# Kernel optimization log

Measured on AMD Instinct MI355X. Metric: run time of the kernel, lower is better.

Reference implementation:

```python
import jax, jax.numpy as jnp
import numpy as np

# ---- Clifford algebra G(3,0,1) (projective GA) blade tables, built once in numpy ----
_BLADES = [(), (0,), (1,), (2,), (3,), (0, 1), (0, 2), (0, 3), (1, 2), (1, 3), (2, 3), (0, 1, 2), (0, 1, 3), (0, 2, 3), (1, 2, 3), (0, 1, 2, 3)]
_IDX = {b: i for i, b in enumerate(_BLADES)}
_METRIC = [0.0, 1.0, 1.0, 1.0]  # e0^2 = 0 (degenerate), e1..e3 square to +1

def _blade_mul(a, b):
    arr = list(a) + list(b)
    sign = 1.0
    swapped = True
    while swapped:  # bubble sort, tracking permutation sign
        swapped = False
        for j in range(len(arr) - 1):
            if arr[j] > arr[j + 1]:
                arr[j], arr[j + 1] = arr[j + 1], arr[j]
                sign = -sign
                swapped = True
    res = []
    j = 0
    while j < len(arr):
        if j + 1 < len(arr) and arr[j] == arr[j + 1]:
            sign *= _METRIC[arr[j]]
            j += 2
        else:
            res.append(arr[j])
            j += 1
    return sign, tuple(res)

_GP = np.zeros((16, 16, 16), np.float32)    # geometric product Cayley table
_WEDGE = np.zeros((16, 16, 16), np.float32)  # outer (wedge) product table
for _i, _a in enumerate(_BLADES):
    for _j, _b in enumerate(_BLADES):
        _s, _r = _blade_mul(_a, _b)
        if _s != 0.0:
            _GP[_i, _j, _IDX[_r]] = _s
        if set(_a).isdisjoint(_b):
            _WEDGE[_i, _j, _IDX[_r]] = _s

# dual = right complement: e_a ^ dual(e_a) = e0123 (metric-free, valid in degenerate PGA)
_D = np.zeros((16, 16), np.float32)
for _i, _a in enumerate(_BLADES):
    _comp = tuple(sorted(set(range(4)) - set(_a)))
    _D[_i, _IDX[_comp]] = _WEDGE[_i, _IDX[_comp], 15]
_UND = np.linalg.inv(_D).astype(np.float32)
# join(x, y) = undual(dual(x) ^ dual(y)) as a single 16^3 trilinear table
_JOIN = np.einsum('ia,jb,abc,ck->ijk', _D, _D, _WEDGE, _UND).astype(np.float32)
_GRADES = np.array([len(b) for b in _BLADES])

GP_T = jnp.asarray(_GP)
JOIN_T = jnp.asarray(_JOIN)
GRADES = jnp.asarray(_GRADES)


def _equilin(x, w):
    # Equivariant linear layer: one channel-mixing matrix per grade.
    # x: [B, N, Cin, 16], w: [5, Cout, Cin] -> [B, N, Cout, 16]
    wk = w[GRADES]  # [16, Cout, Cin]
    return jnp.einsum('bnik,koi->bnok', x, wk)


def setup_inputs() -> dict:
    key = jax.random.key(0)
    ks = jax.random.split(key, 7)
    B, N, Cin, Cout = 32, 1024, 64, 64
    H = Cout // 2
    s_in = 1.0 / np.sqrt(Cin)
    s_out = 1.0 / np.sqrt(Cout)
    return {
        'x': jax.random.normal(ks[0], (B, N, Cin, 16), jnp.float32),
        'ref': jax.random.normal(ks[1], (B, N, 16), jnp.float32),
        'w_prodX': jax.random.normal(ks[2], (5, H, Cin), jnp.float32) * s_in,
        'w_prodY': jax.random.normal(ks[3], (5, H, Cin), jnp.float32) * s_in,
        'w_joinX': jax.random.normal(ks[4], (5, H, Cin), jnp.float32) * s_in,
        'w_joinY': jax.random.normal(ks[5], (5, H, Cin), jnp.float32) * s_in,
        'w_final': jax.random.normal(ks[6], (5, Cout, Cout), jnp.float32) * s_out,
    }


def reference(x, ref, w_prodX, w_prodY, w_joinX, w_joinY, w_final):
    # geometric product branch
    px = _equilin(x, w_prodX)
    py = _equilin(x, w_prodY)
    prod = jnp.einsum('bnci,bncj,ijk->bnck', px, py, GP_T)
    # equivariant join branch, scaled by reference pseudoscalar coefficient (GATr)
    jx = _equilin(x, w_joinX)
    jy = _equilin(x, w_joinY)
    join = jnp.einsum('bnci,bncj,ijk->bnck', jx, jy, JOIN_T)
    join = join * ref[..., 15][..., None, None]
    feats = jnp.concatenate([prod, join], axis=-2)  # [B, N, Cout, 16]
    return _equilin(feats, w_final)
```

## Files before the change

### kernel.cpp

```cpp
#include <hip/hip_runtime.h>
#include <stdint.h>


#define BN 32768
#define PLANE 1160
#define TROW 72

typedef __attribute__((ext_vector_type(8))) short short8;
typedef __attribute__((ext_vector_type(4))) float f32x4;

#define MFMA_BF16 __builtin_amdgcn_mfma_f32_16x16x32_bf16

constexpr int IDX2MASK[16] = {0,1,2,4,8,3,5,9,6,10,12,7,11,13,14,15};
constexpr int MASK2IDX[16] = {0,1,2,5,3,6,8,11,4,7,9,12,10,13,14,15};

struct MulRes { float s; int idx; };

constexpr MulRes blade_mul(int ia, int ib) {
  int arr[8] = {0,0,0,0,0,0,0,0}; int n = 0;
  for (int e = 0; e < 4; ++e) if ((IDX2MASK[ia] >> e) & 1) arr[n++] = e;
  for (int e = 0; e < 4; ++e) if ((IDX2MASK[ib] >> e) & 1) arr[n++] = e;
  float sign = 1.0f;
  bool sw = true;
  while (sw) {
    sw = false;
    for (int j = 0; j + 1 < n; ++j)
      if (arr[j] > arr[j+1]) { int t = arr[j]; arr[j] = arr[j+1]; arr[j+1] = t; sign = -sign; sw = true; }
  }
  int mask = 0; int j = 0;
  while (j < n) {
    if (j + 1 < n && arr[j] == arr[j+1]) { if (arr[j] == 0) sign = 0.0f; j += 2; }
    else { mask |= 1 << arr[j]; ++j; }
  }
  return MulRes{sign, MASK2IDX[mask]};
}

constexpr float dual_sign(int i) {
  return blade_mul(i, MASK2IDX[15 ^ IDX2MASK[i]]).s;
}

struct Tab { float s[16][16]; int k[16][16]; };

constexpr Tab make_gp() {
  Tab t{};
  for (int i = 0; i < 16; ++i)
    for (int j = 0; j < 16; ++j) { MulRes r = blade_mul(i, j); t.s[i][j] = r.s; t.k[i][j] = r.idx; }
  return t;
}

constexpr Tab make_join() {
  Tab t{};
  for (int i = 0; i < 16; ++i)
    for (int j = 0; j < 16; ++j) {
      int ma = 15 ^ IDX2MASK[i], mb = 15 ^ IDX2MASK[j];
      if (ma & mb) { t.s[i][j] = 0.0f; t.k[i][j] = 0; continue; }
      int ia = MASK2IDX[ma], ib = MASK2IDX[mb];
      MulRes w = blade_mul(ia, ib);
      int kk = MASK2IDX[15 ^ IDX2MASK[w.idx]];
      t.s[i][j] = dual_sign(i) * dual_sign(j) * w.s * dual_sign(kk);
      t.k[i][j] = kk;
    }
  return t;
}

constexpr Tab GPT = make_gp();
constexpr Tab JNT = make_join();
constexpr int GRADE[16] = {0,1,1,1,1,2,2,2,2,2,2,3,3,3,3,4};

struct KTab { int cnt[16]; int ti[16][16]; int tj[16][16]; float ts[16][16]; };
constexpr KTab make_ktab(const Tab& t) {
  KTab b{};
  for (int i = 0; i < 16; ++i)
    for (int j = 0; j < 16; ++j) {
      float s = t.s[i][j];
      if (s != 0.f) { int k = t.k[i][j]; int m = b.cnt[k]; b.cnt[k] = m + 1;
                      b.ti[k][m] = i; b.tj[k][m] = j; b.ts[k][m] = s; }
    }
  return b;
}
constexpr KTab GPK = make_ktab(GPT);
constexpr KTab JNK = make_ktab(JNT);

__device__ __forceinline__ uint32_t f2bf(float f){
  union{float f; uint32_t i;} v; v.f = f;
  return (v.i + 0x7fffu + ((v.i >> 16) & 1u)) >> 16;
}

__device__ short g_wpre_b[4 * 5 * 32 * 64];
__device__ short g_wfin_b[5 * 64 * 64];

__global__ void cast_weights(const float* __restrict__ wpx, const float* __restrict__ wpy,
                             const float* __restrict__ wjx, const float* __restrict__ wjy,
                             const float* __restrict__ wf) {
  int idx = blockIdx.x * 256 + threadIdx.x;
  if (idx < 40960) {
    int which = idx / 10240, r = idx % 10240;
    const float* src = (which == 0) ? wpx : (which == 1) ? wpy : (which == 2) ? wjx : wjy;
    g_wpre_b[idx] = (short)f2bf(src[r]);
  } else if (idx < 40960 + 20480) {
    int r = idx - 40960;
    g_wfin_b[r] = (short)f2bf(wf[r]);
  }
}

__global__ __launch_bounds__(256, 2) void gbl_kernel(
    const float* __restrict__ x,
    const float* __restrict__ ref,
    float* __restrict__ out)
{
  __shared__ __align__(16) short ldsb[16 * PLANE];

  const int tid  = threadIdx.x;
  const int w    = tid >> 6;
  const int lane = tid & 63;
  const int n    = lane & 15;
  const int q    = lane >> 4;
  const int t0   = blockIdx.x * 16;

  {
    const int k  = tid & 15;
    const int tt = tid >> 4;
    const float* xr = x + (size_t)(t0 + tt) * 1024 + k;
    #pragma unroll
    for (int ib = 0; ib < 8; ++ib) {
      float v[8];
      #pragma unroll
      for (int j = 0; j < 8; ++j) v[j] = xr[(ib * 8 + j) * 16];
      short8 p;
      #pragma unroll
      for (int j = 0; j < 8; ++j) p[j] = (short)f2bf(v[j]);
      *(short8*)&ldsb[k * PLANE + tt * TROW + ib * 8] = p;
    }
  }
  __syncthreads();

  const int br = w >> 1, nt = w & 1;

  float px[16][4], py[16][4];

  {
    short8 B[5][2];
    #pragma unroll
    for (int g = 0; g < 5; ++g)
      #pragma unroll
      for (int ks = 0; ks < 2; ++ks)
        B[g][ks] = *(short8*)&g_wpre_b[(((br * 2 + 0) * 5 + g) * 32 + nt * 16 + n) * 64 + ks * 32 + q * 8];
    #pragma unroll
    for (int kb = 0; kb < 16; ++kb) {
      short8 a0 = *(short8*)&ldsb[kb * PLANE + n * TROW + 0  + q * 8];
      short8 a1 = *(short8*)&ldsb[kb * PLANE + n * TROW + 32 + q * 8];
      f32x4 acc = {0.f, 0.f, 0.f, 0.f};
      acc = MFMA_BF16(a0, B[GRADE[kb]][0], acc, 0, 0, 0);
      acc = MFMA_BF16(a1, B[GRADE[kb]][1], acc, 0, 0, 0);
      #pragma unroll
      for (int r = 0; r < 4; ++r) px[kb][r] = acc[r];
    }
  }
  {
    short8 B[5][2];
    #pragma unroll
    for (int g = 0; g < 5; ++g)
      #pragma unroll
      for (int ks = 0; ks < 2; ++ks)
        B[g][ks] = *(short8*)&g_wpre_b[(((br * 2 + 1) * 5 + g) * 32 + nt * 16 + n) * 64 + ks * 32 + q * 8];
    #pragma unroll
    for (int kb = 0; kb < 16; ++kb) {
      short8 a0 = *(short8*)&ldsb[kb * PLANE + n * TROW + 0  + q * 8];
      short8 a1 = *(short8*)&ldsb[kb * PLANE + n * TROW + 32 + q * 8];
      f32x4 acc = {0.f, 0.f, 0.f, 0.f};
      acc = MFMA_BF16(a0, B[GRADE[kb]][0], acc, 0, 0, 0);
      acc = MFMA_BF16(a1, B[GRADE[kb]][1], acc, 0, 0, 0);
      #pragma unroll
      for (int r = 0; r < 4; ++r) py[kb][r] = acc[r];
    }
  }

  __syncthreads();

  {
    float rv[4];
    if (br == 1) {
      #pragma unroll
      for (int r = 0; r < 4; ++r) rv[r] = ref[(size_t)(t0 + 4 * q + r) * 16 + 15];
    }
    const int cg = w * 16 + n;
    #pragma unroll
    for (int k = 0; k < 16; ++k) {
      float a[4] = {0.f, 0.f, 0.f, 0.f};
      if (br == 0) {
        #pragma unroll
        for (int m = 0; m < 16; ++m) {
          if (m < GPK.cnt[k]) {
            const int i = GPK.ti[k][m], j = GPK.tj[k][m];
            const bool neg = GPK.ts[k][m] < 0.f;
            #pragma unroll
            for (int r = 0; r < 4; ++r)
              a[r] = fmaf(neg ? -px[i][r] : px[i][r], py[j][r], a[r]);
          }
        }
      } else {
        #pragma unroll
        for (int m = 0; m < 16; ++m) {
          if (m < JNK.cnt[k]) {
            const int i = JNK.ti[k][m], j = JNK.tj[k][m];
            const bool neg = JNK.ts[k][m] < 0.f;
            #pragma unroll
            for (int r = 0; r < 4; ++r)
              a[r] = fmaf(neg ? -px[i][r] : px[i][r], py[j][r], a[r]);
          }
        }
        #pragma unroll
        for (int r = 0; r < 4; ++r) a[r] *= rv[r];
      }
      #pragma unroll
      for (int r = 0; r < 4; ++r)
        ldsb[k * PLANE + (4 * q + r) * TROW + cg] = (short)f2bf(a[r]);
    }
  }
  __syncthreads();

  {
    short8 BF[5][2];
    #pragma unroll
    for (int g = 0; g < 5; ++g)
      #pragma unroll
      for (int ks = 0; ks < 2; ++ks)
        BF[g][ks] = *(short8*)&g_wfin_b[(g * 64 + w * 16 + n) * 64 + ks * 32 + q * 8];

    f32x4 D[16];
    #pragma unroll
    for (int kb = 0; kb < 16; ++kb) {
      short8 a0 = *(short8*)&ldsb[kb * PLANE + n * TROW + 0  + q * 8];
      short8 a1 = *(short8*)&ldsb[kb * PLANE + n * TROW + 32 + q * 8];
      f32x4 acc = {0.f, 0.f, 0.f, 0.f};
      acc = MFMA_BF16(a0, BF[GRADE[kb]][0], acc, 0, 0, 0);
      acc = MFMA_BF16(a1, BF[GRADE[kb]][1], acc, 0, 0, 0);
      D[kb] = acc;
    }

    const int o = w * 16 + n;
    #pragma unroll
    for (int r = 0; r < 4; ++r) {
      const int t = t0 + 4 * q + r;
      float4* op = (float4*)(out + (size_t)t * 1024 + o * 16);
      op[0] = make_float4(D[0][r],  D[1][r],  D[2][r],  D[3][r]);
      op[1] = make_float4(D[4][r],  D[5][r],  D[6][r],  D[7][r]);
      op[2] = make_float4(D[8][r],  D[9][r],  D[10][r], D[11][r]);
      op[3] = make_float4(D[12][r], D[13][r], D[14][r], D[15][r]);
    }
  }
}

extern "C" void kernel_launch(void* const* d_in, const int* in_sizes, int n_in,
                              void* d_out, int out_size, void* d_ws, size_t ws_size,
                              hipStream_t stream) {
  const float* x   = (const float*)d_in[0];
  const float* ref = (const float*)d_in[1];
  const float* wpx = (const float*)d_in[2];
  const float* wpy = (const float*)d_in[3];
  const float* wjx = (const float*)d_in[4];
  const float* wjy = (const float*)d_in[5];
  const float* wfi = (const float*)d_in[6];

  cast_weights<<<240, 256, 0, stream>>>(wpx, wpy, wjx, wjy, wfi);
  gbl_kernel<<<BN / 16, 256, 0, stream>>>(x, ref, (float*)d_out);
}
```

Before: 285.0 us.

## Switch to fp16 MFMA with packed-half bilinear products and swizzled LDS

```diff
diff --git a/kernel.cpp b/kernel.cpp
--- a/kernel.cpp
+++ b/kernel.cpp
@@ -3,13 +3,16 @@
 
 
 #define BN 32768
-#define PLANE 1160
-#define TROW 72
-
-typedef __attribute__((ext_vector_type(8))) short short8;
+
+typedef __attribute__((ext_vector_type(2))) _Float16 h2;
+typedef __attribute__((ext_vector_type(8))) _Float16 h8;
 typedef __attribute__((ext_vector_type(4))) float f32x4;
 
-#define MFMA_BF16 __builtin_amdgcn_mfma_f32_16x16x32_bf16
+#define MFMA_F16 __builtin_amdgcn_mfma_f32_16x16x32_f16
+
+__device__ __forceinline__ h2 pk(float a, float b) {
+  return (h2)__builtin_amdgcn_cvt_pkrtz(a, b);
+}
 
 constexpr int IDX2MASK[16] = {0,1,2,4,8,3,5,9,6,10,12,7,11,13,14,15};
 constexpr int MASK2IDX[16] = {0,1,2,5,3,6,8,11,4,7,9,12,10,13,14,15};
@@ -66,6 +69,7 @@
 constexpr Tab GPT = make_gp();
 constexpr Tab JNT = make_join();
 constexpr int GRADE[16] = {0,1,1,1,1,2,2,2,2,2,2,3,3,3,3,4};
+constexpr int GSTART[6] = {0,1,5,11,15,16};
 
 struct KTab { int cnt[16]; int ti[16][16]; int tj[16][16]; float ts[16][16]; };
 constexpr KTab make_ktab(const Tab& t) {
@@ -81,13 +85,12 @@
 constexpr KTab GPK = make_ktab(GPT);
 constexpr KTab JNK = make_ktab(JNT);
 
-__device__ __forceinline__ uint32_t f2bf(float f){
-  union{float f; uint32_t i;} v; v.f = f;
-  return (v.i + 0x7fffu + ((v.i >> 16) & 1u)) >> 16;
-}
-
-__device__ short g_wpre_b[4 * 5 * 32 * 64];
-__device__ short g_wfin_b[5 * 64 * 64];
+__device__ __forceinline__ int lds_sh(int k, int tok, int s) {
+  return k * 1024 + tok * 64 + (s ^ (((k + tok) & 7) << 3));
+}
+
+__device__ __align__(16) short g_wpre_h[4 * 5 * 32 * 64];
+__device__ __align__(16) short g_wfin_h[5 * 64 * 64];
 
 __global__ void cast_weights(const float* __restrict__ wpx, const float* __restrict__ wpy,
                              const float* __restrict__ wjx, const float* __restrict__ wjy,
@@ -96,19 +99,21 @@
   if (idx < 40960) {
     int which = idx / 10240, r = idx % 10240;
     const float* src = (which == 0) ? wpx : (which == 1) ? wpy : (which == 2) ? wjx : wjy;
-    g_wpre_b[idx] = (short)f2bf(src[r]);
+    _Float16 h = (_Float16)src[r];
+    g_wpre_h[idx] = __builtin_bit_cast(short, h);
   } else if (idx < 40960 + 20480) {
     int r = idx - 40960;
-    g_wfin_b[r] = (short)f2bf(wf[r]);
-  }
-}
-
-__global__ __launch_bounds__(256, 2) void gbl_kernel(
+    _Float16 h = (_Float16)wf[r];
+    g_wfin_h[r] = __builtin_bit_cast(short, h);
+  }
+}
+
+__global__ __launch_bounds__(256, 4) void gbl_kernel(
     const float* __restrict__ x,
     const float* __restrict__ ref,
     float* __restrict__ out)
 {
-  __shared__ __align__(16) short ldsb[16 * PLANE];
+  __shared__ __align__(16) short ldsb[16 * 1024];
 
   const int tid  = threadIdx.x;
   const int w    = tid >> 6;
@@ -116,6 +121,13 @@
   const int n    = lane & 15;
   const int q    = lane >> 4;
   const int t0   = blockIdx.x * 16;
+  const int br   = w >> 1, nt = w & 1;
+
+  float refv[4];
+  if (br == 1) {
+    #pragma unroll
+    for (int r = 0; r < 4; ++r) refv[r] = ref[(size_t)(t0 + 4 * q + r) * 16 + 15];
+  }
 
   {
     const int k  = tid & 15;
@@ -126,76 +138,57 @@
       float v[8];
       #pragma unroll
       for (int j = 0; j < 8; ++j) v[j] = xr[(ib * 8 + j) * 16];
-      short8 p;
-      #pragma unroll
-      for (int j = 0; j < 8; ++j) p[j] = (short)f2bf(v[j]);
-      *(short8*)&ldsb[k * PLANE + tt * TROW + ib * 8] = p;
+      uint32_t u0 = __builtin_bit_cast(uint32_t, pk(v[0], v[1]));
+      uint32_t u1 = __builtin_bit_cast(uint32_t, pk(v[2], v[3]));
+      uint32_t u2 = __builtin_bit_cast(uint32_t, pk(v[4], v[5]));
+      uint32_t u3 = __builtin_bit_cast(uint32_t, pk(v[6], v[7]));
+      uint4 pv = make_uint4(u0, u1, u2, u3);
+      *(uint4*)&ldsb[lds_sh(k, tt, ib * 8)] = pv;
     }
   }
   __syncthreads();
 
-  const int br = w >> 1, nt = w & 1;
-
-  float px[16][4], py[16][4];
-
-  {
-    short8 B[5][2];
-    #pragma unroll
-    for (int g = 0; g < 5; ++g)
-      #pragma unroll
-      for (int ks = 0; ks < 2; ++ks)
-        B[g][ks] = *(short8*)&g_wpre_b[(((br * 2 + 0) * 5 + g) * 32 + nt * 16 + n) * 64 + ks * 32 + q * 8];
-    #pragma unroll
-    for (int kb = 0; kb < 16; ++kb) {
-      short8 a0 = *(short8*)&ldsb[kb * PLANE + n * TROW + 0  + q * 8];
-      short8 a1 = *(short8*)&ldsb[kb * PLANE + n * TROW + 32 + q * 8];
-      f32x4 acc = {0.f, 0.f, 0.f, 0.f};
-      acc = MFMA_BF16(a0, B[GRADE[kb]][0], acc, 0, 0, 0);
-      acc = MFMA_BF16(a1, B[GRADE[kb]][1], acc, 0, 0, 0);
-      #pragma unroll
-      for (int r = 0; r < 4; ++r) px[kb][r] = acc[r];
-    }
-  }
-  {
-    short8 B[5][2];
-    #pragma unroll
-    for (int g = 0; g < 5; ++g)
-      #pragma unroll
-      for (int ks = 0; ks < 2; ++ks)
-        B[g][ks] = *(short8*)&g_wpre_b[(((br * 2 + 1) * 5 + g) * 32 + nt * 16 + n) * 64 + ks * 32 + q * 8];
-    #pragma unroll
-    for (int kb = 0; kb < 16; ++kb) {
-      short8 a0 = *(short8*)&ldsb[kb * PLANE + n * TROW + 0  + q * 8];
-      short8 a1 = *(short8*)&ldsb[kb * PLANE + n * TROW + 32 + q * 8];
-      f32x4 acc = {0.f, 0.f, 0.f, 0.f};
-      acc = MFMA_BF16(a0, B[GRADE[kb]][0], acc, 0, 0, 0);
-      acc = MFMA_BF16(a1, B[GRADE[kb]][1], acc, 0, 0, 0);
-      #pragma unroll
-      for (int r = 0; r < 4; ++r) py[kb][r] = acc[r];
-    }
-  }
-
+  h2 pxh[16][2], pyh[16][2];
+  {
+    #pragma unroll
+    for (int g = 0; g < 5; ++g) {
+      const short* bx = &g_wpre_h[(((br * 2 + 0) * 5 + g) * 32 + nt * 16 + n) * 64 + q * 8];
+      const short* by = &g_wpre_h[(((br * 2 + 1) * 5 + g) * 32 + nt * 16 + n) * 64 + q * 8];
+      h8 Bx0 = *(const h8*)(bx), Bx1 = *(const h8*)(bx + 32);
+      h8 By0 = *(const h8*)(by), By1 = *(const h8*)(by + 32);
+      #pragma unroll
+      for (int kb = GSTART[g]; kb < GSTART[g + 1]; ++kb) {
+        h8 a0 = *(const h8*)&ldsb[lds_sh(kb, n, q * 8)];
+        h8 a1 = *(const h8*)&ldsb[lds_sh(kb, n, 32 + q * 8)];
+        f32x4 ax = {0.f, 0.f, 0.f, 0.f};
+        ax = MFMA_F16(a0, Bx0, ax, 0, 0, 0);
+        ax = MFMA_F16(a1, Bx1, ax, 0, 0, 0);
+        pxh[kb][0] = pk(ax[0], ax[1]);
+        pxh[kb][1] = pk(ax[2], ax[3]);
+        f32x4 ay = {0.f, 0.f, 0.f, 0.f};
+        ay = MFMA_F16(a0, By0, ay, 0, 0, 0);
+        ay = MFMA_F16(a1, By1, ay, 0, 0, 0);
+        pyh[kb][0] = pk(ay[0], ay[1]);
+        pyh[kb][1] = pk(ay[2], ay[3]);
+      }
+    }
+  }
   __syncthreads();
 
   {
-    float rv[4];
-    if (br == 1) {
-      #pragma unroll
-      for (int r = 0; r < 4; ++r) rv[r] = ref[(size_t)(t0 + 4 * q + r) * 16 + 15];
-    }
+    h2 rv0, rv1;
+    if (br == 1) { rv0 = pk(refv[0], refv[1]); rv1 = pk(refv[2], refv[3]); }
     const int cg = w * 16 + n;
     #pragma unroll
     for (int k = 0; k < 16; ++k) {
-      float a[4] = {0.f, 0.f, 0.f, 0.f};
+      h2 a0 = (_Float16)0.0f, a1 = (_Float16)0.0f;
       if (br == 0) {
         #pragma unroll
         for (int m = 0; m < 16; ++m) {
           if (m < GPK.cnt[k]) {
             const int i = GPK.ti[k][m], j = GPK.tj[k][m];
-            const bool neg = GPK.ts[k][m] < 0.f;
-            #pragma unroll
-            for (int r = 0; r < 4; ++r)
-              a[r] = fmaf(neg ? -px[i][r] : px[i][r], py[j][r], a[r]);
+            if (GPK.ts[k][m] < 0.f) { a0 -= pxh[i][0] * pyh[j][0]; a1 -= pxh[i][1] * pyh[j][1]; }
+            else                    { a0 += pxh[i][0] * pyh[j][0]; a1 += pxh[i][1] * pyh[j][1]; }
           }
         }
       } else {
@@ -203,50 +196,49 @@
         for (int m = 0; m < 16; ++m) {
           if (m < JNK.cnt[k]) {
             const int i = JNK.ti[k][m], j = JNK.tj[k][m];
-            const bool neg = JNK.ts[k][m] < 0.f;
-            #pragma unroll
-            for (int r = 0; r < 4; ++r)
-              a[r] = fmaf(neg ? -px[i][r] : px[i][r], py[j][r], a[r]);
+            if (JNK.ts[k][m] < 0.f) { a0 -= pxh[i][0] * pyh[j][0]; a1 -= pxh[i][1] * pyh[j][1]; }
+            else                    { a0 += pxh[i][0] * pyh[j][0]; a1 += pxh[i][1] * pyh[j][1]; }
           }
         }
-        #pragma unroll
-        for (int r = 0; r < 4; ++r) a[r] *= rv[r];
-      }
-      #pragma unroll
-      for (int r = 0; r < 4; ++r)
-        ldsb[k * PLANE + (4 * q + r) * TROW + cg] = (short)f2bf(a[r]);
+        a0 *= rv0; a1 *= rv1;
+      }
+      uint32_t u0 = __builtin_bit_cast(uint32_t, a0);
+      uint32_t u1 = __builtin_bit_cast(uint32_t, a1);
+      ldsb[lds_sh(k, 4 * q + 0, cg)] = (short)(u0 & 0xffffu);
+      ldsb[lds_sh(k, 4 * q + 1, cg)] = (short)(u0 >> 16);
+      ldsb[lds_sh(k, 4 * q + 2, cg)] = (short)(u1 & 0xffffu);
+      ldsb[lds_sh(k, 4 * q + 3, cg)] = (short)(u1 >> 16);
     }
   }
   __syncthreads();
 
   {
-    short8 BF[5][2];
-    #pragma unroll
-    for (int g = 0; g < 5; ++g)
-      #pragma unroll
-      for (int ks = 0; ks < 2; ++ks)
-        BF[g][ks] = *(short8*)&g_wfin_b[(g * 64 + w * 16 + n) * 64 + ks * 32 + q * 8];
-
-    f32x4 D[16];
-    #pragma unroll
-    for (int kb = 0; kb < 16; ++kb) {
-      short8 a0 = *(short8*)&ldsb[kb * PLANE + n * TROW + 0  + q * 8];
-      short8 a1 = *(short8*)&ldsb[kb * PLANE + n * TROW + 32 + q * 8];
-      f32x4 acc = {0.f, 0.f, 0.f, 0.f};
-      acc = MFMA_BF16(a0, BF[GRADE[kb]][0], acc, 0, 0, 0);
-      acc = MFMA_BF16(a1, BF[GRADE[kb]][1], acc, 0, 0, 0);
-      D[kb] = acc;
-    }
-
     const int o = w * 16 + n;
-    #pragma unroll
-    for (int r = 0; r < 4; ++r) {
-      const int t = t0 + 4 * q + r;
-      float4* op = (float4*)(out + (size_t)t * 1024 + o * 16);
-      op[0] = make_float4(D[0][r],  D[1][r],  D[2][r],  D[3][r]);
-      op[1] = make_float4(D[4][r],  D[5][r],  D[6][r],  D[7][r]);
-      op[2] = make_float4(D[8][r],  D[9][r],  D[10][r], D[11][r]);
-      op[3] = make_float4(D[12][r], D[13][r], D[14][r], D[15][r]);
+    h8 BF0, BF1;
+    #pragma unroll
+    for (int gb = 0; gb < 4; ++gb) {
+      f32x4 Dg[4];
+      #pragma unroll
+      for (int kk = 0; kk < 4; ++kk) {
+        const int kb = gb * 4 + kk;
+        if (kb == 0 || kb == 1 || kb == 5 || kb == 11 || kb == 15) {
+          const short* bf = &g_wfin_h[(GRADE[kb] * 64 + o) * 64 + q * 8];
+          BF0 = *(const h8*)(bf);
+          BF1 = *(const h8*)(bf + 32);
+        }
+        h8 a0 = *(const h8*)&ldsb[lds_sh(kb, n, q * 8)];
+        h8 a1 = *(const h8*)&ldsb[lds_sh(kb, n, 32 + q * 8)];
+        f32x4 acc = {0.f, 0.f, 0.f, 0.f};
+        acc = MFMA_F16(a0, BF0, acc, 0, 0, 0);
+        acc = MFMA_F16(a1, BF1, acc, 0, 0, 0);
+        Dg[kk] = acc;
+      }
+      #pragma unroll
+      for (int r = 0; r < 4; ++r) {
+        const int t = t0 + 4 * q + r;
+        *(float4*)(out + (size_t)t * 1024 + o * 16 + gb * 4) =
+            make_float4(Dg[0][r], Dg[1][r], Dg[2][r], Dg[3][r]);
+      }
     }
   }
 }
```

After: 306.6 us. 7.6% more time.
